# Kernel optimization log

Measured on AMD Instinct MI355X. Metric: run time of the kernel, lower is better.

Reference implementation:

```python
import jax, jax.numpy as jnp
import numpy as np


def setup_inputs() -> dict:
    key = jax.random.key(0)
    ks = jax.random.split(key, 5)
    S, B, E, H = 512, 64, 1024, 1024
    scale = 0.02
    return {
        "x": jax.random.normal(ks[0], (S, B, E), dtype=jnp.float32),
        "W_all": jax.random.normal(ks[1], (4 * H, E + H), dtype=jnp.float32) * scale,
        "b_all": jnp.zeros((4 * H,), dtype=jnp.float32),
        "Q": jax.random.normal(ks[2], (E, H), dtype=jnp.float32) * scale,
        "R": jax.random.normal(ks[3], (H, E), dtype=jnp.float32) * scale,
        "mog_iters": 5,
    }


def reference(x, W_all, b_all, Q, R, mog_iters):
    # x: [S, B, E] (length-first). Returns (outputs [S,B,H], (ht, ct)).
    S, B, E = x.shape
    H = W_all.shape[0] // 4

    def step(carry, xt):
        ht, ct = carry
        # Mogrifier rounds (odd rounds update x, even rounds update h)
        for i in range(1, mog_iters + 1):
            if i % 2:
                xt = 2.0 * jax.nn.sigmoid(ht @ Q.T) * xt
            else:
                ht = 2.0 * jax.nn.sigmoid(xt @ R.T) * ht
        z = jnp.concatenate([xt, ht], axis=-1) @ W_all.T + b_all  # [B, 4H]
        i_g, f_g, g_g, o_g = jnp.split(z, 4, axis=-1)
        ct = jax.nn.sigmoid(f_g) * ct + jax.nn.sigmoid(i_g) * jnp.tanh(g_g)
        ht = jax.nn.sigmoid(o_g) * jnp.tanh(ct)
        return (ht, ct), ht

    h0 = jnp.zeros((B, H), dtype=x.dtype)
    c0 = jnp.zeros((B, H), dtype=x.dtype)
    (ht, ct), outputs = jax.lax.scan(step, (h0, c0), x)
    return outputs, (ht, ct)
```

## Files before the change

### kernel.cpp

```cpp
#include <hip/hip_runtime.h>
#include <hip/hip_bf16.h>
#include <math.h>


using bf16   = __bf16;
using bf16x8 = __attribute__((ext_vector_type(8))) __bf16;
using f32x4  = __attribute__((ext_vector_type(4))) float;

#define MFMA16(a,b,c) __builtin_amdgcn_mfma_f32_16x16x32_bf16((a),(b),(c),0,0,0)

__device__ __forceinline__ float fsig(float x) { return 1.f / (1.f + expf(-x)); }

__device__ __forceinline__ void split8(const float* __restrict__ p,
                                       bf16x8& ah, bf16x8& al) {
  f32x4 v0 = *(const f32x4*)p;
  f32x4 v1 = *(const f32x4*)(p + 4);
#pragma unroll
  for (int e = 0; e < 4; ++e) {
    bf16 h0 = (bf16)v0[e]; ah[e] = h0;     al[e] = (bf16)(v0[e] - (float)h0);
    bf16 h1 = (bf16)v1[e]; ah[4 + e] = h1; al[4 + e] = (bf16)(v1[e] - (float)h1);
  }
}

__global__ void prep(const float* __restrict__ Q, const float* __restrict__ R,
                     bf16* __restrict__ Qh, bf16* __restrict__ Ql,
                     bf16* __restrict__ Rh, bf16* __restrict__ Rl,
                     float* __restrict__ nM, float* __restrict__ cM) {
  const long tid = (long)blockIdx.x * blockDim.x + threadIdx.x;
  const long nth = (long)gridDim.x * blockDim.x;
  for (long i = tid; i < 1024L * 1024 / 4; i += nth) {
    float4 v = ((const float4*)Q)[i];
    bf16 a0 = (bf16)v.x, a1 = (bf16)v.y, a2 = (bf16)v.z, a3 = (bf16)v.w;
    Qh[i*4+0] = a0; Qh[i*4+1] = a1; Qh[i*4+2] = a2; Qh[i*4+3] = a3;
    Ql[i*4+0] = (bf16)(v.x - (float)a0); Ql[i*4+1] = (bf16)(v.y - (float)a1);
    Ql[i*4+2] = (bf16)(v.z - (float)a2); Ql[i*4+3] = (bf16)(v.w - (float)a3);
    float4 u = ((const float4*)R)[i];
    bf16 b0 = (bf16)u.x, b1 = (bf16)u.y, b2 = (bf16)u.z, b3 = (bf16)u.w;
    Rh[i*4+0] = b0; Rh[i*4+1] = b1; Rh[i*4+2] = b2; Rh[i*4+3] = b3;
    Rl[i*4+0] = (bf16)(u.x - (float)b0); Rl[i*4+1] = (bf16)(u.y - (float)b1);
    Rl[i*4+2] = (bf16)(u.z - (float)b2); Rl[i*4+3] = (bf16)(u.w - (float)b3);
  }
  for (long i = tid; i < 64L * 1024; i += nth) {
    nM[i] = 0.f; cM[i] = 0.f;
  }
}

__global__ __launch_bounds__(512) void mog_phase(
    const float* __restrict__ Af, const bf16* __restrict__ Bh,
    const bf16* __restrict__ Bl, const float* __restrict__ mult,
    float* __restrict__ dstM) {
  __shared__ f32x4 red[7][64];
  const int mt = blockIdx.x >> 6, c = blockIdx.x & 63;
  const int tid = threadIdx.x, l = tid & 63, w = tid >> 6;
  const int r16 = l & 15, kg = l >> 4;
  const size_t kb = (size_t)w * 128 + kg * 8;
  const bf16*  bhp = Bh + (size_t)(16 * c + r16) * 1024 + kb;
  const bf16*  blp = Bl + (size_t)(16 * c + r16) * 1024 + kb;
  const float* afp = Af + (size_t)(16 * mt + r16) * 1024 + kb;
  f32x4 acc = {};
#pragma unroll
  for (int ks = 0; ks < 4; ++ks) {
    bf16x8 bh = *(const bf16x8*)(bhp + ks * 32);
    bf16x8 bl = *(const bf16x8*)(blp + ks * 32);
    bf16x8 ah, al;
    split8(afp + ks * 32, ah, al);
    acc = MFMA16(al, bl, acc);
    acc = MFMA16(al, bh, acc);
    acc = MFMA16(ah, bl, acc);
    acc = MFMA16(ah, bh, acc);
  }
  if (w) red[w - 1][l] = acc;
  __syncthreads();
  if (w == 0) {
#pragma unroll
    for (int kk = 0; kk < 7; ++kk) acc += red[kk][l];
    const int col = 16 * c + r16;
#pragma unroll
    for (int q = 0; q < 4; ++q) {
      const int row = 16 * mt + kg * 4 + q;
      const size_t idx = (size_t)row * 1024 + col;
      dstM[idx] = 2.f * fsig(acc[q]) * mult[idx];
    }
  }
}

__global__ __launch_bounds__(512) void gate4(
    const float* __restrict__ xMf, const float* __restrict__ hMf,
    const float* __restrict__ Wf, const float* __restrict__ ball,
    float* __restrict__ cM, float* __restrict__ nM,
    float* __restrict__ out, int t) {
  __shared__ f32x4 red[8][4][64];
  const int g = blockIdx.x;
  const int tid = threadIdx.x, l = tid & 63, w = tid >> 6;
  const int r16 = l & 15, kg = l >> 4;
  const float* Abf = (w < 4) ? xMf : hMf;
  const size_t kb = (size_t)(w & 3) * 256 + kg * 8;
  const size_t wrow = (size_t)(r16 >> 2) * 1024 + 4 * g + (r16 & 3);
  const float* wp = Wf + wrow * 2048 + (size_t)w * 256 + kg * 8;
  f32x4 acc[4] = {};
#pragma unroll
  for (int ks = 0; ks < 8; ++ks) {
    bf16x8 bh, bl;
    split8(wp + ks * 32, bh, bl);
#pragma unroll
    for (int m = 0; m < 4; ++m) {
      bf16x8 ah, al;
      split8(Abf + (size_t)(16 * m + r16) * 1024 + kb + ks * 32, ah, al);
      acc[m] = MFMA16(al, bl, acc[m]);
      acc[m] = MFMA16(al, bh, acc[m]);
      acc[m] = MFMA16(ah, bl, acc[m]);
      acc[m] = MFMA16(ah, bh, acc[m]);
    }
  }
#pragma unroll
  for (int m = 0; m < 4; ++m) red[w][m][l] = acc[m];
  __syncthreads();
  if (tid < 256) {
    const int row = tid >> 2, hc = tid & 3;
    const int m = row >> 4, rem = row & 15;
    const int kgq = rem >> 2, q = rem & 3;
    const int hcg = 4 * g + hc;
    float z[4];
#pragma unroll
    for (int gg = 0; gg < 4; ++gg) {
      const int lane = kgq * 16 + gg * 4 + hc;
      float s = red[0][m][lane][q];
#pragma unroll
      for (int kk = 1; kk < 8; ++kk) s += red[kk][m][lane][q];
      z[gg] = s + ball[gg * 1024 + hcg];
    }
    const size_t idx = (size_t)row * 1024 + hcg;
    const float cc = fsig(z[1]) * cM[idx] + fsig(z[0]) * tanhf(z[2]);
    const float hh = fsig(z[3]) * tanhf(cc);
    cM[idx] = cc;
    nM[idx] = hh;
    out[(size_t)t * 65536 + idx] = hh;
    if (t == 511) {
      out[(size_t)512 * 65536 + idx] = hh;
      out[(size_t)512 * 65536 + 65536 + idx] = cc;
    }
  }
}

extern "C" void kernel_launch(void* const* d_in, const int* in_sizes, int n_in,
                              void* d_out, int out_size, void* d_ws, size_t ws_size,
                              hipStream_t stream) {
  (void)in_sizes; (void)n_in; (void)out_size; (void)ws_size;
  const float* x    = (const float*)d_in[0];
  const float* Wall = (const float*)d_in[1];
  const float* ball = (const float*)d_in[2];
  const float* Q    = (const float*)d_in[3];
  const float* R    = (const float*)d_in[4];
  float* out = (float*)d_out;

  char* ws = (char*)d_ws;
  size_t off = 0;
  bf16* Qh = (bf16*)(ws + off); off += (size_t)1024 * 1024 * 2;
  bf16* Ql = (bf16*)(ws + off); off += (size_t)1024 * 1024 * 2;
  bf16* Rh = (bf16*)(ws + off); off += (size_t)1024 * 1024 * 2;
  bf16* Rl = (bf16*)(ws + off); off += (size_t)1024 * 1024 * 2;
  float* xM = (float*)(ws + off); off += (size_t)64 * 1024 * 4;
  float* hM = (float*)(ws + off); off += (size_t)64 * 1024 * 4;
  float* nM = (float*)(ws + off); off += (size_t)64 * 1024 * 4;
  float* cM = (float*)(ws + off); off += (size_t)64 * 1024 * 4;

  prep<<<512, 256, 0, stream>>>(Q, R, Qh, Ql, Rh, Rl, nM, cM);
  for (int t = 0; t < 512; ++t) {
    const float* xt = x + (size_t)t * 65536;
    mog_phase<<<256, 512, 0, stream>>>(nM, Qh, Ql, xt, xM);
    mog_phase<<<256, 512, 0, stream>>>(xM, Rh, Rl, nM, hM);
    mog_phase<<<256, 512, 0, stream>>>(hM, Qh, Ql, xM, xM);
    mog_phase<<<256, 512, 0, stream>>>(xM, Rh, Rl, hM, hM);
    mog_phase<<<256, 512, 0, stream>>>(hM, Qh, Ql, xM, xM);
    gate4<<<256, 512, 0, stream>>>(xM, hM, Wall, ball, cM, nM, out, t);
  }
}
```

Baseline: 27.02 ms.

## Double gate4 column tile per block and prefetch next timestep input into staging buffer

gate4 now computes 8 hidden columns per block (128 blocks instead of 256), so each A-operand split of xM/hM is reused across two weight tiles. The goal is to halve the redundant A loads and conversions. gate4 also copies the next timestep's x slice into a workspace staging buffer, which the first mogrifier phase then reads, aiming to move x into cache-friendly memory ahead of time. The cost is fewer blocks, which means lower occupancy on a 256-CU device, and doubled shared memory for the reduction.

```diff
diff --git a/kernel.cpp b/kernel.cpp
--- a/kernel.cpp
+++ b/kernel.cpp
@@ -23,9 +23,11 @@
 }
 
 __global__ void prep(const float* __restrict__ Q, const float* __restrict__ R,
+                     const float* __restrict__ xin,
                      bf16* __restrict__ Qh, bf16* __restrict__ Ql,
                      bf16* __restrict__ Rh, bf16* __restrict__ Rl,
-                     float* __restrict__ nM, float* __restrict__ cM) {
+                     float* __restrict__ nM, float* __restrict__ cM,
+                     float* __restrict__ xstage) {
   const long tid = (long)blockIdx.x * blockDim.x + threadIdx.x;
   const long nth = (long)gridDim.x * blockDim.x;
   for (long i = tid; i < 1024L * 1024 / 4; i += nth) {
@@ -42,6 +44,7 @@
   }
   for (long i = tid; i < 64L * 1024; i += nth) {
     nM[i] = 0.f; cM[i] = 0.f;
+    xstage[i] = xin[i];
   }
 }
 
@@ -88,45 +91,62 @@
     const float* __restrict__ xMf, const float* __restrict__ hMf,
     const float* __restrict__ Wf, const float* __restrict__ ball,
     float* __restrict__ cM, float* __restrict__ nM,
+    const float* __restrict__ xin_next, float* __restrict__ xstage,
     float* __restrict__ out, int t) {
-  __shared__ f32x4 red[8][4][64];
+  __shared__ f32x4 red[8][8][64];
   const int g = blockIdx.x;
   const int tid = threadIdx.x, l = tid & 63, w = tid >> 6;
   const int r16 = l & 15, kg = l >> 4;
+
+  if (t < 511) {
+    const int si = g * 512 + tid;
+    xstage[si] = xin_next[si];
+  }
+
   const float* Abf = (w < 4) ? xMf : hMf;
   const size_t kb = (size_t)(w & 3) * 256 + kg * 8;
-  const size_t wrow = (size_t)(r16 >> 2) * 1024 + 4 * g + (r16 & 3);
-  const float* wp = Wf + wrow * 2048 + (size_t)w * 256 + kg * 8;
-  f32x4 acc[4] = {};
+  const size_t wr0 = (size_t)(r16 >> 2) * 1024 + 8 * g + (r16 & 3);
+  const float* wp0 = Wf + wr0 * 2048       + (size_t)w * 256 + kg * 8;
+  const float* wp1 = Wf + (wr0 + 4) * 2048 + (size_t)w * 256 + kg * 8;
+  f32x4 acc[4][2] = {};
 #pragma unroll
   for (int ks = 0; ks < 8; ++ks) {
-    bf16x8 bh, bl;
-    split8(wp + ks * 32, bh, bl);
+    bf16x8 bh0, bl0, bh1, bl1;
+    split8(wp0 + ks * 32, bh0, bl0);
+    split8(wp1 + ks * 32, bh1, bl1);
 #pragma unroll
     for (int m = 0; m < 4; ++m) {
       bf16x8 ah, al;
       split8(Abf + (size_t)(16 * m + r16) * 1024 + kb + ks * 32, ah, al);
-      acc[m] = MFMA16(al, bl, acc[m]);
-      acc[m] = MFMA16(al, bh, acc[m]);
-      acc[m] = MFMA16(ah, bl, acc[m]);
-      acc[m] = MFMA16(ah, bh, acc[m]);
+      acc[m][0] = MFMA16(al, bl0, acc[m][0]);
+      acc[m][0] = MFMA16(al, bh0, acc[m][0]);
+      acc[m][0] = MFMA16(ah, bl0, acc[m][0]);
+      acc[m][0] = MFMA16(ah, bh0, acc[m][0]);
+      acc[m][1] = MFMA16(al, bl1, acc[m][1]);
+      acc[m][1] = MFMA16(al, bh1, acc[m][1]);
+      acc[m][1] = MFMA16(ah, bl1, acc[m][1]);
+      acc[m][1] = MFMA16(ah, bh1, acc[m][1]);
     }
   }
 #pragma unroll
-  for (int m = 0; m < 4; ++m) red[w][m][l] = acc[m];
+  for (int m = 0; m < 4; ++m) {
+    red[w][m * 2 + 0][l] = acc[m][0];
+    red[w][m * 2 + 1][l] = acc[m][1];
+  }
   __syncthreads();
-  if (tid < 256) {
-    const int row = tid >> 2, hc = tid & 3;
+  {
+    const int row = tid >> 3, hc = tid & 7;
     const int m = row >> 4, rem = row & 15;
     const int kgq = rem >> 2, q = rem & 3;
-    const int hcg = 4 * g + hc;
+    const int n = hc >> 2, j4 = hc & 3;
+    const int hcg = 8 * g + hc;
     float z[4];
 #pragma unroll
     for (int gg = 0; gg < 4; ++gg) {
-      const int lane = kgq * 16 + gg * 4 + hc;
-      float s = red[0][m][lane][q];
+      const int lane = kgq * 16 + gg * 4 + j4;
+      float s = red[0][m * 2 + n][lane][q];
 #pragma unroll
-      for (int kk = 1; kk < 8; ++kk) s += red[kk][m][lane][q];
+      for (int kk = 1; kk < 8; ++kk) s += red[kk][m * 2 + n][lane][q];
       z[gg] = s + ball[gg * 1024 + hcg];
     }
     const size_t idx = (size_t)row * 1024 + hcg;
@@ -163,15 +183,17 @@
   float* hM = (float*)(ws + off); off += (size_t)64 * 1024 * 4;
   float* nM = (float*)(ws + off); off += (size_t)64 * 1024 * 4;
   float* cM = (float*)(ws + off); off += (size_t)64 * 1024 * 4;
+  float* xstage = (float*)(ws + off); off += (size_t)64 * 1024 * 4;
 
-  prep<<<512, 256, 0, stream>>>(Q, R, Qh, Ql, Rh, Rl, nM, cM);
+  prep<<<512, 256, 0, stream>>>(Q, R, x, Qh, Ql, Rh, Rl, nM, cM, xstage);
   for (int t = 0; t < 512; ++t) {
-    const float* xt = x + (size_t)t * 65536;
-    mog_phase<<<256, 512, 0, stream>>>(nM, Qh, Ql, xt, xM);
+    mog_phase<<<256, 512, 0, stream>>>(nM, Qh, Ql, xstage, xM);
     mog_phase<<<256, 512, 0, stream>>>(xM, Rh, Rl, nM, hM);
     mog_phase<<<256, 512, 0, stream>>>(hM, Qh, Ql, xM, xM);
     mog_phase<<<256, 512, 0, stream>>>(xM, Rh, Rl, hM, hM);
     mog_phase<<<256, 512, 0, stream>>>(hM, Qh, Ql, xM, xM);
-    gate4<<<256, 512, 0, stream>>>(xM, hM, Wall, ball, cM, nM, out, t);
+    gate4<<<128, 512, 0, stream>>>(xM, hM, Wall, ball, cM, nM,
+                                   x + (size_t)(t + 1) * 65536, xstage,
+                                   out, t);
   }
 }
```

Result: slower. 28.34 ms (+4.9%).

## Overlap h-half of gate GEMM with final mogrifier round in one launch

Applied to the files above, without the earlier changes.

Splits the gate matmul into h and x halves. The h half runs in the same launch as the fifth mogrifier round because both depend only on the final h. The x half then finishes in a lighter gate kernel that adds the stored partial from a global buffer. This shortens the per-step critical path at the cost of an extra global round trip for the partial gate sums.

```diff
diff --git a/kernel.cpp b/kernel.cpp
--- a/kernel.cpp
+++ b/kernel.cpp
@@ -45,13 +45,13 @@
   }
 }
 
-__global__ __launch_bounds__(512) void mog_phase(
+__device__ __forceinline__ void mog_body(
+    int mt, int c, int tid, char* smem,
     const float* __restrict__ Af, const bf16* __restrict__ Bh,
     const bf16* __restrict__ Bl, const float* __restrict__ mult,
     float* __restrict__ dstM) {
-  __shared__ f32x4 red[7][64];
-  const int mt = blockIdx.x >> 6, c = blockIdx.x & 63;
-  const int tid = threadIdx.x, l = tid & 63, w = tid >> 6;
+  f32x4* red = (f32x4*)smem;
+  const int l = tid & 63, w = tid >> 6;
   const int r16 = l & 15, kg = l >> 4;
   const size_t kb = (size_t)w * 128 + kg * 8;
   const bf16*  bhp = Bh + (size_t)(16 * c + r16) * 1024 + kb;
@@ -69,11 +69,11 @@
     acc = MFMA16(ah, bl, acc);
     acc = MFMA16(ah, bh, acc);
   }
-  if (w) red[w - 1][l] = acc;
+  if (w) red[(w - 1) * 64 + l] = acc;
   __syncthreads();
   if (w == 0) {
 #pragma unroll
-    for (int kk = 0; kk < 7; ++kk) acc += red[kk][l];
+    for (int kk = 0; kk < 7; ++kk) acc += red[kk * 64 + l];
     const int col = 16 * c + r16;
 #pragma unroll
     for (int q = 0; q < 4; ++q) {
@@ -84,22 +84,26 @@
   }
 }
 
-__global__ __launch_bounds__(512) void gate4(
-    const float* __restrict__ xMf, const float* __restrict__ hMf,
-    const float* __restrict__ Wf, const float* __restrict__ ball,
-    float* __restrict__ cM, float* __restrict__ nM,
-    float* __restrict__ out, int t) {
-  __shared__ f32x4 red[8][4][64];
-  const int g = blockIdx.x;
-  const int tid = threadIdx.x, l = tid & 63, w = tid >> 6;
+__global__ __launch_bounds__(512) void mog_phase(
+    const float* __restrict__ Af, const bf16* __restrict__ Bh,
+    const bf16* __restrict__ Bl, const float* __restrict__ mult,
+    float* __restrict__ dstM) {
+  __shared__ __align__(16) char smem[7 * 64 * 16];
+  mog_body(blockIdx.x >> 6, blockIdx.x & 63, threadIdx.x, smem,
+           Af, Bh, Bl, mult, dstM);
+}
+
+__device__ __forceinline__ void halfgate_body(
+    int g, int tid, f32x4* red, const float* __restrict__ Abf,
+    const float* __restrict__ Wf, int khalf) {
+  const int l = tid & 63, w = tid >> 6;
   const int r16 = l & 15, kg = l >> 4;
-  const float* Abf = (w < 4) ? xMf : hMf;
-  const size_t kb = (size_t)(w & 3) * 256 + kg * 8;
+  const size_t kb = (size_t)w * 128 + kg * 8;
   const size_t wrow = (size_t)(r16 >> 2) * 1024 + 4 * g + (r16 & 3);
-  const float* wp = Wf + wrow * 2048 + (size_t)w * 256 + kg * 8;
+  const float* wp = Wf + wrow * 2048 + (size_t)khalf * 1024 + kb;
   f32x4 acc[4] = {};
 #pragma unroll
-  for (int ks = 0; ks < 8; ++ks) {
+  for (int ks = 0; ks < 4; ++ks) {
     bf16x8 bh, bl;
     split8(wp + ks * 32, bh, bl);
 #pragma unroll
@@ -113,8 +117,48 @@
     }
   }
 #pragma unroll
-  for (int m = 0; m < 4; ++m) red[w][m][l] = acc[m];
+  for (int m = 0; m < 4; ++m) red[(w * 4 + m) * 64 + l] = acc[m];
   __syncthreads();
+}
+
+__global__ __launch_bounds__(512) void mog5_zh(
+    const float* __restrict__ hMf,
+    const bf16* __restrict__ Qh, const bf16* __restrict__ Ql,
+    float* __restrict__ xM,
+    const float* __restrict__ Wf, float* __restrict__ zbuf) {
+  __shared__ __align__(16) char smem[8 * 4 * 64 * 16];
+  const int bid = blockIdx.x, tid = threadIdx.x;
+  if (bid < 256) {
+    mog_body(bid >> 6, bid & 63, tid, smem, hMf, Qh, Ql, xM, xM);
+    return;
+  }
+  const int g = bid - 256;
+  f32x4* red = (f32x4*)smem;
+  halfgate_body(g, tid, red, hMf, Wf, 1);
+  if (tid < 256) {
+    const int row = tid >> 2, hc = tid & 3;
+    const int m = row >> 4, rem = row & 15;
+    const int kgq = rem >> 2, q = rem & 3;
+#pragma unroll
+    for (int gg = 0; gg < 4; ++gg) {
+      const int lane = kgq * 16 + gg * 4 + hc;
+      float s = red[(0 * 4 + m) * 64 + lane][q];
+#pragma unroll
+      for (int kk = 1; kk < 8; ++kk) s += red[(kk * 4 + m) * 64 + lane][q];
+      zbuf[(size_t)row * 4096 + gg * 1024 + 4 * g + hc] = s;
+    }
+  }
+}
+
+__global__ __launch_bounds__(512) void gate_x(
+    const float* __restrict__ xMf,
+    const float* __restrict__ Wf, const float* __restrict__ zbuf,
+    const float* __restrict__ ball, float* __restrict__ cM,
+    float* __restrict__ nM, float* __restrict__ out, int t) {
+  __shared__ __align__(16) char smem[8 * 4 * 64 * 16];
+  const int g = blockIdx.x, tid = threadIdx.x;
+  f32x4* red = (f32x4*)smem;
+  halfgate_body(g, tid, red, xMf, Wf, 0);
   if (tid < 256) {
     const int row = tid >> 2, hc = tid & 3;
     const int m = row >> 4, rem = row & 15;
@@ -124,10 +168,11 @@
 #pragma unroll
     for (int gg = 0; gg < 4; ++gg) {
       const int lane = kgq * 16 + gg * 4 + hc;
-      float s = red[0][m][lane][q];
-#pragma unroll
-      for (int kk = 1; kk < 8; ++kk) s += red[kk][m][lane][q];
-      z[gg] = s + ball[gg * 1024 + hcg];
+      float s = red[(0 * 4 + m) * 64 + lane][q];
+#pragma unroll
+      for (int kk = 1; kk < 8; ++kk) s += red[(kk * 4 + m) * 64 + lane][q];
+      z[gg] = s + zbuf[(size_t)row * 4096 + gg * 1024 + hcg]
+                + ball[gg * 1024 + hcg];
     }
     const size_t idx = (size_t)row * 1024 + hcg;
     const float cc = fsig(z[1]) * cM[idx] + fsig(z[0]) * tanhf(z[2]);
@@ -163,6 +208,7 @@
   float* hM = (float*)(ws + off); off += (size_t)64 * 1024 * 4;
   float* nM = (float*)(ws + off); off += (size_t)64 * 1024 * 4;
   float* cM = (float*)(ws + off); off += (size_t)64 * 1024 * 4;
+  float* zbuf = (float*)(ws + off); off += (size_t)64 * 4096 * 4;
 
   prep<<<512, 256, 0, stream>>>(Q, R, Qh, Ql, Rh, Rl, nM, cM);
   for (int t = 0; t < 512; ++t) {
@@ -171,7 +217,7 @@
     mog_phase<<<256, 512, 0, stream>>>(xM, Rh, Rl, nM, hM);
     mog_phase<<<256, 512, 0, stream>>>(hM, Qh, Ql, xM, xM);
     mog_phase<<<256, 512, 0, stream>>>(xM, Rh, Rl, hM, hM);
-    mog_phase<<<256, 512, 0, stream>>>(hM, Qh, Ql, xM, xM);
-    gate4<<<256, 512, 0, stream>>>(xM, hM, Wall, ball, cM, nM, out, t);
-  }
-}
+    mog5_zh<<<512, 512, 0, stream>>>(hM, Qh, Ql, xM, Wall, zbuf);
+    gate_x<<<256, 512, 0, stream>>>(xM, Wall, zbuf, ball, cM, nM, out, t);
+  }
+}
```

New measurement: 27.76 ms. +2.7%, slower.
